# Performance work log

Measured on AMD Instinct MI355X. Metric: run time of the kernel, lower is better.

## Reference

```python
import jax, jax.numpy as jnp
import numpy as np

B, N, DIM, H, DH, MLP, DEPTH = 32, 256, 384, 6, 64, 1536, 12
INNER = H * DH
LN_EPS = 1e-5
LS_INIT = 0.1  # LayerScale init_eps for depth <= 18


def setup_inputs() -> dict:
    key = jax.random.key(0)
    ks = jax.random.split(key, 10)
    f = lambda k, shape, s=0.02: jax.random.normal(k, shape, jnp.float32) * s
    return {
        "x": jax.random.normal(ks[0], (B, N, DIM), jnp.float32),
        "ln1_g": jnp.ones((DEPTH, DIM), jnp.float32),
        "ln1_b": jnp.zeros((DEPTH, DIM), jnp.float32),
        "wq": f(ks[1], (DEPTH, DIM, INNER)),
        "wkv": f(ks[2], (DEPTH, DIM, 2 * INNER)),
        "scale": jnp.full((DEPTH, H), DH ** -0.5, jnp.float32),  # learned per-head scale
        "mix_pre": f(ks[3], (DEPTH, H, H), 1.0),   # torch.randn init
        "mix_post": f(ks[4], (DEPTH, H, H), 1.0),
        "wo": f(ks[5], (DEPTH, INNER, DIM)),
        "bo": jnp.zeros((DEPTH, DIM), jnp.float32),
        "ls1": jnp.full((DEPTH, DIM), LS_INIT, jnp.float32),
        "ln2_g": jnp.ones((DEPTH, DIM), jnp.float32),
        "ln2_b": jnp.zeros((DEPTH, DIM), jnp.float32),
        "w1": f(ks[6], (DEPTH, DIM, MLP)),
        "b1": jnp.zeros((DEPTH, MLP), jnp.float32),
        "w2": f(ks[7], (DEPTH, MLP, DIM)),
        "b2": jnp.zeros((DEPTH, DIM), jnp.float32),
        "ls2": jnp.full((DEPTH, DIM), LS_INIT, jnp.float32),
    }


def _layernorm(x, g, b):
    mu = jnp.mean(x, axis=-1, keepdims=True)
    var = jnp.mean(jnp.square(x - mu), axis=-1, keepdims=True)
    return (x - mu) * jax.lax.rsqrt(var + LN_EPS) * g + b


def reference(x, ln1_g, ln1_b, wq, wkv, scale, mix_pre, mix_post, wo, bo, ls1,
              ln2_g, ln2_b, w1, b1, w2, b2, ls2):
    diag = jnp.eye(N, dtype=bool)  # self-attention diagonal mask

    def block(x, p):
        (g1, bb1, wq_, wkv_, sc, mp, mq, wo_, bo_, l1,
         g2, bb2, w1_, b1_, w2_, b2_, l2) = p
        # --- talking-heads attention (PreNorm + LayerScale + residual) ---
        y = _layernorm(x, g1, bb1)
        q = (y @ wq_).reshape(B, N, H, DH).transpose(0, 2, 1, 3)       # b h n d
        kv = y @ wkv_
        k, v = jnp.split(kv, 2, axis=-1)
        k = k.reshape(B, N, H, DH).transpose(0, 2, 1, 3)
        v = v.reshape(B, N, H, DH).transpose(0, 2, 1, 3)
        dots = jnp.einsum('bhid,bhjd->bhij', q, k) * sc[None, :, None, None]
        dots = jnp.einsum('bhij,hg->bgij', dots, mp)                   # pre-softmax head mix
        dots = jnp.where(diag, -jnp.inf, dots)                         # mask self positions
        attn = jax.nn.softmax(dots, axis=-1)
        attn = jnp.einsum('bhij,hg->bgij', attn, mq)                   # post-softmax head mix
        o = jnp.einsum('bhij,bhjd->bhid', attn, v)
        o = o.transpose(0, 2, 1, 3).reshape(B, N, INNER) @ wo_ + bo_
        x = o * l1 + x
        # --- FFN (PreNorm + LayerScale + residual) ---
        y2 = _layernorm(x, g2, bb2)
        h = jax.nn.gelu(y2 @ w1_ + b1_, approximate=False)
        x = (h @ w2_ + b2_) * l2 + x
        return x, None

    params = (ln1_g, ln1_b, wq, wkv, scale, mix_pre, mix_post, wo, bo, ls1,
              ln2_g, ln2_b, w1, b1, w2, b2, ls2)
    x, _ = jax.lax.scan(block, x, params)
    return x
```

## Files before the change

kernel.cpp:

```cpp
#include <hip/hip_runtime.h>
#include <hip/hip_bf16.h>
#include <math.h>

#define B_ 32
#define N_ 256
#define DIM_ 384
#define H_ 6
#define DH_ 64
#define INNER_ 384
#define MLP_ 1536
#define DEPTH_ 12
#define T_ (B_ * N_)

typedef __bf16 bf16x8 __attribute__((ext_vector_type(8)));
typedef __bf16 bf16x4 __attribute__((ext_vector_type(4)));
typedef float f32x4 __attribute__((ext_vector_type(4)));

typedef const __attribute__((address_space(1))) void* gas_ptr;
typedef __attribute__((address_space(3))) void* las_ptr;

#define WQKV_OFF 0
#define WO_OFF   (1152 * 384)
#define W1_OFF   (WO_OFF + 384 * 384)
#define W2_OFF   (W1_OFF + 1536 * 384)
#define WBUF_ELEMS (W2_OFF + 384 * 1536)

__global__ __launch_bounds__(256) void convert_w_all(
    const float* __restrict__ wq0, const float* __restrict__ wkv0,
    const float* __restrict__ wo0, const float* __restrict__ w10,
    const float* __restrict__ w20, __bf16* __restrict__ wbuf0)
{
    __shared__ float til[64][65];
    int t = blockIdx.x;
    int l = t / 432; t -= l * 432;
    const float* wq  = wq0  + (size_t)l * DIM_ * INNER_;
    const float* wkv = wkv0 + (size_t)l * DIM_ * 2 * INNER_;
    const float* wo  = wo0  + (size_t)l * INNER_ * DIM_;
    const float* w1  = w10  + (size_t)l * DIM_ * MLP_;
    const float* w2  = w20  + (size_t)l * MLP_ * DIM_;
    __bf16* wbuf = wbuf0 + (size_t)l * WBUF_ELEMS;

    int lane = threadIdx.x & 63, seg = threadIdx.x >> 6;
    const float* src; __bf16* dst;
    int Ns, sc, dK, dR, k0;
    if (t < 108) {
        int nt = t / 6, kt = t % 6;
        int n0 = nt * 64; k0 = kt * 64;
        dst = wbuf + WQKV_OFF; dK = 384; dR = n0;
        if (n0 < 384) { src = wq;  Ns = 384; sc = n0; }
        else          { src = wkv; Ns = 768; sc = n0 - 384; }
    } else if (t < 144) {
        int u = t - 108; int nt = u / 6, kt = u % 6;
        src = wo; Ns = 384; sc = nt * 64;
        dst = wbuf + WO_OFF; dK = 384; dR = nt * 64; k0 = kt * 64;
    } else if (t < 288) {
        int u = t - 144; int nt = u / 6, kt = u % 6;
        src = w1; Ns = 1536; sc = nt * 64;
        dst = wbuf + W1_OFF; dK = 384; dR = nt * 64; k0 = kt * 64;
    } else {
        int u = t - 288; int nt = u / 24, kt = u % 24;
        src = w2; Ns = 384; sc = nt * 64;
        dst = wbuf + W2_OFF; dK = 1536; dR = nt * 64; k0 = kt * 64;
    }
    #pragma unroll
    for (int r = 0; r < 16; ++r) {
        int i = seg * 16 + r;
        til[i][lane] = src[(size_t)(k0 + i) * Ns + sc + lane];
    }
    __syncthreads();
    #pragma unroll
    for (int r = 0; r < 16; ++r) {
        int i = seg * 16 + r;
        dst[(size_t)(dR + i) * dK + k0 + lane] = (__bf16)til[lane][i];
    }
}

__global__ __launch_bounds__(64) void ln1w(
    const float* __restrict__ x, const float* __restrict__ g,
    const float* __restrict__ b, __bf16* __restrict__ y)
{
    size_t row = blockIdx.x;
    int lane = threadIdx.x;
    const float* xr = x + row * DIM_;
    float v[6];
    #pragma unroll
    for (int s = 0; s < 6; ++s) v[s] = xr[lane + 64 * s];
    float sum = 0.f;
    #pragma unroll
    for (int s = 0; s < 6; ++s) sum += v[s];
    #pragma unroll
    for (int o = 32; o > 0; o >>= 1) sum += __shfl_xor(sum, o);
    float mu = sum * (1.0f / DIM_);
    float var = 0.f;
    #pragma unroll
    for (int s = 0; s < 6; ++s) { float d = v[s] - mu; var += d * d; }
    #pragma unroll
    for (int o = 32; o > 0; o >>= 1) var += __shfl_xor(var, o);
    float rs = rsqrtf(var * (1.0f / DIM_) + 1e-5f);
    __bf16* yr = y + row * DIM_;
    #pragma unroll
    for (int s = 0; s < 6; ++s) {
        int e = lane + 64 * s;
        yr[e] = (__bf16)((v[s] - mu) * rs * g[e] + b[e]);
    }
}

template<int MODE, int K, int BM, int BN>
__global__ __launch_bounds__(256) void gemmt(
    const __bf16* __restrict__ A, const __bf16* __restrict__ Bt,
    const float* __restrict__ bias, const float* __restrict__ ls,
    float* __restrict__ xf, __bf16* __restrict__ out,
    __bf16* __restrict__ oq, __bf16* __restrict__ ok, __bf16* __restrict__ ov,
    int Nn)
{
    constexpr int WM = BM / 32, WN = BN / 32;
    constexpr int MT = T_ / BM;
    constexpr int nIter = K / 32;
    __shared__ __align__(16) __bf16 sA[2][BM * 32];
    __shared__ __align__(16) __bf16 sB[2][BN * 32];

    int id = blockIdx.x;
    int nxg = (int)gridDim.x >> 3;
    int wg = (id & 7) * nxg + (id >> 3);
    int bm = (wg & (MT - 1)) * BM;
    int bn = (wg / MT) * BN;
    int tid = threadIdx.x;
    int lane = tid & 63, wid = tid >> 6;
    int wm = (wid & 1) * (BM / 2), wn = (wid >> 1) * (BN / 2);
    int fm = lane & 15, fq = lane >> 4;

    f32x4 acc[WM][WN] = {};

    const __bf16* aBase = A + (size_t)(bm + wid * 16 + (lane >> 2)) * K + (lane & 3) * 8;
    const __bf16* bBase = Bt + (size_t)(bn + wid * 16 + (lane >> 2)) * K + (lane & 3) * 8;

    auto stage = [&](int buf, int kk) {
        #pragma unroll
        for (int qI = 0; qI < BM / 64; ++qI)
            __builtin_amdgcn_global_load_lds(
                (gas_ptr)(aBase + (size_t)qI * 64 * K + kk),
                (las_ptr)&sA[buf][qI * 2048 + wid * 512], 16, 0, 0);
        #pragma unroll
        for (int qI = 0; qI < BN / 64; ++qI)
            __builtin_amdgcn_global_load_lds(
                (gas_ptr)(bBase + (size_t)qI * 64 * K + kk),
                (las_ptr)&sB[buf][qI * 2048 + wid * 512], 16, 0, 0);
    };

    stage(0, 0);
    __syncthreads();

    #pragma unroll
    for (int i = 0; i < nIter; ++i) {
        int cur = i & 1;
        if (i + 1 < nIter) stage(cur ^ 1, (i + 1) * 32);
        bf16x8 af[WM], bfr[WN];
        #pragma unroll
        for (int ii = 0; ii < WM; ++ii)
            af[ii] = *(const bf16x8*)&sA[cur][(wm + ii * 16 + fm) * 32 + fq * 8];
        #pragma unroll
        for (int jj = 0; jj < WN; ++jj)
            bfr[jj] = *(const bf16x8*)&sB[cur][(wn + jj * 16 + fm) * 32 + fq * 8];
        #pragma unroll
        for (int ii = 0; ii < WM; ++ii)
            #pragma unroll
            for (int jj = 0; jj < WN; ++jj)
                acc[ii][jj] = __builtin_amdgcn_mfma_f32_16x16x32_bf16(af[ii], bfr[jj], acc[ii][jj], 0, 0, 0);
        if (i + 1 < nIter) __syncthreads();
    }

    #pragma unroll
    for (int jj = 0; jj < WN; ++jj) {
        int col = bn + wn + jj * 16 + fm;
        float bv = (MODE != 0) ? bias[col] : 0.0f;
        float lv = (MODE == 2) ? ls[col] : 0.0f;
        #pragma unroll
        for (int ii = 0; ii < WM; ++ii) {
            #pragma unroll
            for (int r = 0; r < 4; ++r) {
                int row = bm + wm + ii * 16 + fq * 4 + r;
                float v = acc[ii][jj][r];
                if (MODE == 0) {
                    if (col < 384)      oq[(size_t)row * 384 + col] = (__bf16)v;
                    else if (col < 768) ok[(size_t)row * 384 + col - 384] = (__bf16)v;
                    else {
                        int bb = row >> 8, tj = row & 255;
                        ov[((size_t)bb * 384 + (col - 768)) * 256 + tj] = (__bf16)v;
                    }
                } else if (MODE == 1) {
                    v += bv;
                    v = 0.5f * v * (1.0f + erff(v * 0.70710678118f));
                    out[(size_t)row * Nn + col] = (__bf16)v;
                } else {
                    size_t idx = (size_t)row * Nn + col;
                    xf[idx] = (v + bv) * lv + xf[idx];
                }
            }
        }
    }
}

#define PAD_S 264

__global__ __launch_bounds__(384) void attn_mfma(
    const __bf16* __restrict__ q, const __bf16* __restrict__ kb,
    const __bf16* __restrict__ vT, const float* __restrict__ scale,
    const float* __restrict__ mp, const float* __restrict__ mq,
    __bf16* __restrict__ o)
{
    __shared__ __bf16 sbuf[96][PAD_S];

    int id = blockIdx.x;
    int b = (id & 7) + ((id >> 3) & 3) * 8;
    int i0 = (id >> 5) * 16;
    int tid = threadIdx.x;
    int lane = tid & 63, wid = tid >> 6;
    int fm = lane & 15, fq = lane >> 4;

    int h = wid;
    bf16x8 qf[2];
    #pragma unroll
    for (int ks = 0; ks < 2; ++ks)
        qf[ks] = *(const bf16x8*)&q[(size_t)(b * 256 + i0 + fm) * 384 + h * 64 + ks * 32 + fq * 8];
    #pragma unroll 4
    for (int jt = 0; jt < 16; ++jt) {
        f32x4 a = {};
        #pragma unroll
        for (int ks = 0; ks < 2; ++ks) {
            bf16x8 bfr = *(const bf16x8*)&kb[(size_t)(b * 256 + jt * 16 + fm) * 384 + h * 64 + ks * 32 + fq * 8];
            a = __builtin_amdgcn_mfma_f32_16x16x32_bf16(qf[ks], bfr, a, 0, 0, 0);
        }
        #pragma unroll
        for (int r = 0; r < 4; ++r)
            sbuf[h * 16 + fq * 4 + r][jt * 16 + fm] = (__bf16)a[r];
    }

    float mps[36], mqs[36];
    #pragma unroll
    for (int t = 0; t < 36; ++t) { mps[t] = mp[t] * scale[t / 6]; mqs[t] = mq[t]; }

    __syncthreads();

    for (int i = wid; i < 16; i += 6) {
        float sv[6][4];
        #pragma unroll
        for (int h2 = 0; h2 < 6; ++h2) {
            bf16x4 v4 = *(const bf16x4*)&sbuf[h2 * 16 + i][lane * 4];
            #pragma unroll
            for (int c = 0; c < 4; ++c) sv[h2][c] = (float)v4[c];
        }
        int drow = i0 + i;
        float pv[6][4];
        #pragma unroll
        for (int g2 = 0; g2 < 6; ++g2) {
            float t0[4];
            #pragma unroll
            for (int c = 0; c < 4; ++c) {
                float r2 = 0.f;
                #pragma unroll
                for (int h2 = 0; h2 < 6; ++h2) r2 += sv[h2][c] * mps[h2 * 6 + g2];
                t0[c] = (lane * 4 + c == drow) ? -1e30f : r2;
            }
            float m = fmaxf(fmaxf(t0[0], t0[1]), fmaxf(t0[2], t0[3]));
            #pragma unroll
            for (int off = 32; off > 0; off >>= 1) m = fmaxf(m, __shfl_xor(m, off));
            float e0 = __expf(t0[0] - m), e1 = __expf(t0[1] - m);
            float e2 = __expf(t0[2] - m), e3 = __expf(t0[3] - m);
            float s = e0 + e1 + e2 + e3;
            #pragma unroll
            for (int off = 32; off > 0; off >>= 1) s += __shfl_xor(s, off);
            float inv = 1.0f / s;
            pv[g2][0] = e0 * inv; pv[g2][1] = e1 * inv;
            pv[g2][2] = e2 * inv; pv[g2][3] = e3 * inv;
        }
        #pragma unroll
        for (int g2 = 0; g2 < 6; ++g2) {
            bf16x4 w4;
            #pragma unroll
            for (int c = 0; c < 4; ++c) {
                float r2 = 0.f;
                #pragma unroll
                for (int h2 = 0; h2 < 6; ++h2) r2 += pv[h2][c] * mqs[h2 * 6 + g2];
                w4[c] = (__bf16)r2;
            }
            *(bf16x4*)&sbuf[g2 * 16 + i][lane * 4] = w4;
        }
    }
    __syncthreads();

    int gg = wid;
    f32x4 acco[4] = {};
    #pragma unroll
    for (int jc = 0; jc < 4; ++jc) {
        #pragma unroll
        for (int ks = 0; ks < 2; ++ks) {
            bf16x8 af = *(const bf16x8*)&sbuf[gg * 16 + fm][jc * 64 + ks * 32 + fq * 8];
            #pragma unroll
            for (int nt = 0; nt < 4; ++nt) {
                bf16x8 bfr = *(const bf16x8*)&vT[(size_t)(b * 384 + gg * 64 + nt * 16 + fm) * 256 + jc * 64 + ks * 32 + fq * 8];
                acco[nt] = __builtin_amdgcn_mfma_f32_16x16x32_bf16(af, bfr, acco[nt], 0, 0, 0);
            }
        }
    }
    #pragma unroll
    for (int nt = 0; nt < 4; ++nt)
        #pragma unroll
        for (int r = 0; r < 4; ++r)
            o[(size_t)(b * 256 + i0 + fq * 4 + r) * 384 + gg * 64 + nt * 16 + fm] = (__bf16)acco[nt][r];
}

extern "C" void kernel_launch(void* const* d_in, const int* in_sizes, int n_in,
                              void* d_out, int out_size, void* d_ws, size_t ws_size,
                              hipStream_t stream) {
    const float* x      = (const float*)d_in[0];
    const float* ln1_g  = (const float*)d_in[1];
    const float* ln1_b  = (const float*)d_in[2];
    const float* wq     = (const float*)d_in[3];
    const float* wkv    = (const float*)d_in[4];
    const float* scale  = (const float*)d_in[5];
    const float* mixp   = (const float*)d_in[6];
    const float* mixq   = (const float*)d_in[7];
    const float* wo     = (const float*)d_in[8];
    const float* bo     = (const float*)d_in[9];
    const float* ls1    = (const float*)d_in[10];
    const float* ln2_g  = (const float*)d_in[11];
    const float* ln2_b  = (const float*)d_in[12];
    const float* w1     = (const float*)d_in[13];
    const float* b1     = (const float*)d_in[14];
    const float* w2     = (const float*)d_in[15];
    const float* b2     = (const float*)d_in[16];
    const float* ls2    = (const float*)d_in[17];

    char* ws = (char*)d_ws;
    float*  xf = (float*)ws;                      ws += (size_t)T_ * DIM_ * 4;
    __bf16* y  = (__bf16*)ws;                     ws += (size_t)T_ * DIM_ * 2;
    __bf16* q  = (__bf16*)ws;                     ws += (size_t)T_ * DIM_ * 2;
    __bf16* kb = (__bf16*)ws;                     ws += (size_t)T_ * DIM_ * 2;
    __bf16* vT = (__bf16*)ws;                     ws += (size_t)T_ * DIM_ * 2;
    __bf16* o  = (__bf16*)ws;                     ws += (size_t)T_ * DIM_ * 2;
    __bf16* wbuf = (__bf16*)ws;                   ws += (size_t)WBUF_ELEMS * DEPTH_ * 2;
    __bf16* h  = q;

    size_t nBytes = (size_t)T_ * DIM_ * sizeof(float);
    hipMemcpyAsync(xf, x, nBytes, hipMemcpyDeviceToDevice, stream);

    convert_w_all<<<432 * DEPTH_, 256, 0, stream>>>(wq, wkv, wo, w1, w2, wbuf);

    for (int l = 0; l < DEPTH_; ++l) {
        __bf16* wl = wbuf + (size_t)l * WBUF_ELEMS;

        ln1w<<<T_, 64, 0, stream>>>(xf, ln1_g + (size_t)l * DIM_, ln1_b + (size_t)l * DIM_, y);

        gemmt<0, 384, 128, 128><<<64 * 9, 256, 0, stream>>>(
            y, wl + WQKV_OFF, nullptr, nullptr, nullptr, nullptr,
            q, kb, vT, 1152);

        attn_mfma<<<512, 384, 0, stream>>>(
            q, kb, vT, scale + (size_t)l * H_,
            mixp + (size_t)l * H_ * H_, mixq + (size_t)l * H_ * H_, o);

        gemmt<2, 384, 64, 64><<<128 * 6, 256, 0, stream>>>(
            o, wl + WO_OFF, bo + (size_t)l * DIM_, ls1 + (size_t)l * DIM_,
            xf, nullptr, nullptr, nullptr, nullptr, DIM_);

        ln1w<<<T_, 64, 0, stream>>>(xf, ln2_g + (size_t)l * DIM_, ln2_b + (size_t)l * DIM_, y);

        gemmt<1, 384, 128, 128><<<64 * 12, 256, 0, stream>>>(
            y, wl + W1_OFF, b1 + (size_t)l * MLP_, nullptr,
            nullptr, h, nullptr, nullptr, nullptr, MLP_);

        gemmt<2, 1536, 64, 64><<<128 * 6, 256, 0, stream>>>(
            h, wl + W2_OFF, b2 + (size_t)l * DIM_, ls2 + (size_t)l * DIM_,
            xf, nullptr, nullptr, nullptr, nullptr, DIM_);
    }

    hipMemcpyAsync(d_out, xf, nBytes, hipMemcpyDeviceToDevice, stream);
}
```

Before: 2.012 ms.

## Add BK=64 K-tiles with XOR-swizzled LDS and N-major tile ordering

The GEMM template gains a K-tile depth parameter. The two 64x64 GEMMs (Wo and W2) now use BK=64 with an XOR swizzle on LDS columns, which halves the number of barriers per K and should avoid LDS bank conflicts. Tile-to-block mapping also changes so that consecutive workgroups walk N tiles within the same M tile (NT constant), aiming at better reuse of A rows in cache. The cost is larger LDS buffers per block for the BK=64 variants and more fragment registers.

```diff
diff --git a/kernel.cpp b/kernel.cpp
--- a/kernel.cpp
+++ b/kernel.cpp
@@ -105,7 +105,7 @@
     }
 }
 
-template<int MODE, int K, int BM, int BN>
+template<int MODE, int K, int BM, int BN, int BK, int NT>
 __global__ __launch_bounds__(256) void gemmt(
     const __bf16* __restrict__ A, const __bf16* __restrict__ Bt,
     const float* __restrict__ bias, const float* __restrict__ ls,
@@ -114,16 +114,21 @@
     int Nn)
 {
     constexpr int WM = BM / 32, WN = BN / 32;
+    constexpr int KS = BK / 32;
     constexpr int MT = T_ / BM;
-    constexpr int nIter = K / 32;
-    __shared__ __align__(16) __bf16 sA[2][BM * 32];
-    __shared__ __align__(16) __bf16 sB[2][BN * 32];
+    constexpr int nIter = K / BK;
+    constexpr bool SWZ = (BK == 64);
+    constexpr int RPI = 512 / BK;
+    constexpr int CL  = BK / 8;
+
+    __shared__ __align__(16) __bf16 sA[2][BM * BK];
+    __shared__ __align__(16) __bf16 sB[2][BN * BK];
 
     int id = blockIdx.x;
-    int nxg = (int)gridDim.x >> 3;
+    constexpr int nxg = (MT * NT) / 8;
     int wg = (id & 7) * nxg + (id >> 3);
-    int bm = (wg & (MT - 1)) * BM;
-    int bn = (wg / MT) * BN;
+    int bm = (wg / NT) * BM;
+    int bn = (wg % NT) * BN;
     int tid = threadIdx.x;
     int lane = tid & 63, wid = tid >> 6;
     int wm = (wid & 1) * (BM / 2), wn = (wid >> 1) * (BN / 2);
@@ -131,19 +136,21 @@
 
     f32x4 acc[WM][WN] = {};
 
-    const __bf16* aBase = A + (size_t)(bm + wid * 16 + (lane >> 2)) * K + (lane & 3) * 8;
-    const __bf16* bBase = Bt + (size_t)(bn + wid * 16 + (lane >> 2)) * K + (lane & 3) * 8;
+    int lr = lane / CL, lc = lane % CL;
+    int lcs = SWZ ? (lc ^ lr) : lc;
+    const __bf16* aBase = A + (size_t)(bm + wid * RPI + lr) * K + lcs * 8;
+    const __bf16* bBase = Bt + (size_t)(bn + wid * RPI + lr) * K + lcs * 8;
 
     auto stage = [&](int buf, int kk) {
         #pragma unroll
-        for (int qI = 0; qI < BM / 64; ++qI)
+        for (int qI = 0; qI < BM / (4 * RPI); ++qI)
             __builtin_amdgcn_global_load_lds(
-                (gas_ptr)(aBase + (size_t)qI * 64 * K + kk),
+                (gas_ptr)(aBase + (size_t)(qI * 4 * RPI) * K + kk),
                 (las_ptr)&sA[buf][qI * 2048 + wid * 512], 16, 0, 0);
         #pragma unroll
-        for (int qI = 0; qI < BN / 64; ++qI)
+        for (int qI = 0; qI < BN / (4 * RPI); ++qI)
             __builtin_amdgcn_global_load_lds(
-                (gas_ptr)(bBase + (size_t)qI * 64 * K + kk),
+                (gas_ptr)(bBase + (size_t)(qI * 4 * RPI) * K + kk),
                 (las_ptr)&sB[buf][qI * 2048 + wid * 512], 16, 0, 0);
     };
 
@@ -153,19 +160,31 @@
     #pragma unroll
     for (int i = 0; i < nIter; ++i) {
         int cur = i & 1;
-        if (i + 1 < nIter) stage(cur ^ 1, (i + 1) * 32);
-        bf16x8 af[WM], bfr[WN];
-        #pragma unroll
-        for (int ii = 0; ii < WM; ++ii)
-            af[ii] = *(const bf16x8*)&sA[cur][(wm + ii * 16 + fm) * 32 + fq * 8];
-        #pragma unroll
-        for (int jj = 0; jj < WN; ++jj)
-            bfr[jj] = *(const bf16x8*)&sB[cur][(wn + jj * 16 + fm) * 32 + fq * 8];
-        #pragma unroll
-        for (int ii = 0; ii < WM; ++ii)
-            #pragma unroll
-            for (int jj = 0; jj < WN; ++jj)
-                acc[ii][jj] = __builtin_amdgcn_mfma_f32_16x16x32_bf16(af[ii], bfr[jj], acc[ii][jj], 0, 0, 0);
+        if (i + 1 < nIter) stage(cur ^ 1, (i + 1) * BK);
+        bf16x8 af[KS][WM], bfr[KS][WN];
+        #pragma unroll
+        for (int ks = 0; ks < KS; ++ks) {
+            #pragma unroll
+            for (int ii = 0; ii < WM; ++ii) {
+                int row = wm + ii * 16 + fm;
+                int c = SWZ ? (((ks * 4 + fq) ^ (row & 7)) * 8) : (ks * 32 + fq * 8);
+                af[ks][ii] = *(const bf16x8*)&sA[cur][row * BK + c];
+            }
+            #pragma unroll
+            for (int jj = 0; jj < WN; ++jj) {
+                int row = wn + jj * 16 + fm;
+                int c = SWZ ? (((ks * 4 + fq) ^ (row & 7)) * 8) : (ks * 32 + fq * 8);
+                bfr[ks][jj] = *(const bf16x8*)&sB[cur][row * BK + c];
+            }
+        }
+        #pragma unroll
+        for (int ks = 0; ks < KS; ++ks)
+            #pragma unroll
+            for (int ii = 0; ii < WM; ++ii)
+                #pragma unroll
+                for (int jj = 0; jj < WN; ++jj)
+                    acc[ii][jj] = __builtin_amdgcn_mfma_f32_16x16x32_bf16(
+                        af[ks][ii], bfr[ks][jj], acc[ii][jj], 0, 0, 0);
         if (i + 1 < nIter) __syncthreads();
     }
 
@@ -351,7 +370,7 @@
 
         ln1w<<<T_, 64, 0, stream>>>(xf, ln1_g + (size_t)l * DIM_, ln1_b + (size_t)l * DIM_, y);
 
-        gemmt<0, 384, 128, 128><<<64 * 9, 256, 0, stream>>>(
+        gemmt<0, 384, 128, 128, 32, 9><<<576, 256, 0, stream>>>(
             y, wl + WQKV_OFF, nullptr, nullptr, nullptr, nullptr,
             q, kb, vT, 1152);
 
@@ -359,17 +378,17 @@
             q, kb, vT, scale + (size_t)l * H_,
             mixp + (size_t)l * H_ * H_, mixq + (size_t)l * H_ * H_, o);
 
-        gemmt<2, 384, 64, 64><<<128 * 6, 256, 0, stream>>>(
+        gemmt<2, 384, 64, 64, 64, 6><<<768, 256, 0, stream>>>(
             o, wl + WO_OFF, bo + (size_t)l * DIM_, ls1 + (size_t)l * DIM_,
             xf, nullptr, nullptr, nullptr, nullptr, DIM_);
 
         ln1w<<<T_, 64, 0, stream>>>(xf, ln2_g + (size_t)l * DIM_, ln2_b + (size_t)l * DIM_, y);
 
-        gemmt<1, 384, 128, 128><<<64 * 12, 256, 0, stream>>>(
+        gemmt<1, 384, 128, 128, 32, 12><<<768, 256, 0, stream>>>(
             y, wl + W1_OFF, b1 + (size_t)l * MLP_, nullptr,
             nullptr, h, nullptr, nullptr, nullptr, MLP_);
 
-        gemmt<2, 1536, 64, 64><<<128 * 6, 256, 0, stream>>>(
+        gemmt<2, 1536, 64, 64, 64, 6><<<768, 256, 0, stream>>>(
             h, wl + W2_OFF, b2 + (size_t)l * DIM_, ls2 + (size_t)l * DIM_,
             xf, nullptr, nullptr, nullptr, nullptr, DIM_);
     }
```

After: 1.726 ms. 14.2% less time.
